# Kernel tuning notes

Hardware: AMD Instinct MI355X
Metric: run time of the kernel (lower is better)

## Reference

```python
import jax, jax.numpy as jnp
import numpy as np

K = 3
TOPK = 10
HORIZON = 12


def gru_cell(x, h, w_ih, w_hh, b_ih, b_hh):
    # torch GRU gate order: r, z, n ; n = tanh(W_in x + b_in + r*(W_hn h + b_hn))
    gx = x @ w_ih.T + b_ih
    gh = h @ w_hh.T + b_hh
    H = h.shape[-1]
    r = jax.nn.sigmoid(gx[:, :H] + gh[:, :H])
    z = jax.nn.sigmoid(gx[:, H:2 * H] + gh[:, H:2 * H])
    n = jnp.tanh(gx[:, 2 * H:] + r * gh[:, 2 * H:])
    return (1.0 - z) * n + z * h


def setup_inputs() -> dict:
    key = jax.random.key(0)
    ks = jax.random.split(key, 16)
    B, T, N, F = 128, 12, 207, 14
    H = 128
    f = lambda i, shp, s=0.1: jax.random.normal(ks[i], shp, dtype=jnp.float32) * s
    return {
        'x': jax.random.normal(ks[0], (B, T, N, F), dtype=jnp.float32),
        'A_physical': jax.random.uniform(ks[1], (N, N), dtype=jnp.float32),
        'fc_start_w': f(2, (16, 1), 0.5),
        'fc_start_b': jnp.zeros((16,), jnp.float32),
        'alpha': jnp.float32(0.5),
        'context_w': f(3, (32, 13)),
        'context_b': jnp.zeros((32,), jnp.float32),
        'tcn_w': f(4, (64, 1, 1, 3), 0.3),
        'tcn_b': jnp.zeros((64,), jnp.float32),
        'theta': f(5, (K, 32, 32), 0.15),
        'attn_w': f(6, (1, 65)),
        'attn_b': jnp.zeros((1,), jnp.float32),
        'enc_w_ih': f(7, (3 * H, 65)),
        'enc_w_hh': f(8, (3 * H, H)),
        'enc_b_ih': jnp.zeros((3 * H,), jnp.float32),
        'enc_b_hh': jnp.zeros((3 * H,), jnp.float32),
        'dec_w_ih': f(9, (3 * H, 33)),
        'dec_w_hh': f(10, (3 * H, H)),
        'dec_b_ih': jnp.zeros((3 * H,), jnp.float32),
        'dec_b_hh': jnp.zeros((3 * H,), jnp.float32),
        'out_w': f(11, (1, H)),
        'out_b': jnp.zeros((1,), jnp.float32),
    }


def reference(x, A_physical, fc_start_w, fc_start_b, alpha, context_w, context_b,
              tcn_w, tcn_b, theta, attn_w, attn_b,
              enc_w_ih, enc_w_hh, enc_b_ih, enc_b_hh,
              dec_w_ih, dec_w_hh, dec_b_ih, dec_b_hh, out_w, out_b):
    B, T, N, _ = x.shape
    H = enc_w_hh.shape[1]
    traffic = x[..., 0:1]          # [B,T,N,1]
    context = x[..., 1:]           # [B,T,N,13]

    # ---- dynamic graph: topk + scatter + softmax, blended with physical ----
    state = traffic[:, -1]                                   # [B,N,1]
    emb = jnp.tanh(state @ fc_start_w.T + fc_start_b)        # [B,N,16]
    A_dyn = jax.nn.relu(jnp.einsum('bnd,bmd->bnm', emb, emb))
    vals, idx = jax.lax.top_k(A_dyn, TOPK)
    sparse = jnp.zeros_like(A_dyn).at[
        jnp.arange(B)[:, None, None], jnp.arange(N)[None, :, None], idx].set(vals)
    A_dyn = jax.nn.softmax(sparse, axis=2)
    a = jax.nn.sigmoid(alpha)
    A = a * A_physical[None] + (1.0 - a) * A_dyn             # [B,N,N]

    # ---- gated temporal conv (causal, GLU) ----
    xt = jnp.transpose(traffic, (0, 3, 2, 1))                # [B,1,N,T]
    conv = jax.lax.conv_general_dilated(
        xt, tcn_w, (1, 1), [(0, 0), (2, 0)],
        dimension_numbers=('NCHW', 'OIHW', 'NCHW')) + tcn_b[None, :, None, None]
    P, Q = jnp.split(conv, 2, axis=1)
    t_feat = jnp.transpose(P * jax.nn.sigmoid(Q), (0, 3, 2, 1))  # [B,T,N,32]

    # ---- Chebyshev K-hop graph conv ----
    I = jnp.eye(N, dtype=x.dtype)
    lam = jnp.clip(jnp.max(jnp.sum(A, -1), -1), 1.0)[:, None, None]
    L = 2.0 * A / lam - I[None]
    Tk = [jnp.broadcast_to(I[None], (B, N, N)), L]
    for k in range(2, K):
        Tk.append(2.0 * jnp.einsum('bnm,bmp->bnp', L, Tk[-1]) - Tk[-2])
    s = 0.0
    for k in range(K):
        rhs = jnp.einsum('btnf,fo->btno', t_feat, theta[k])
        s = s + jnp.einsum('bnm,btmo->btno', Tk[k], rhs)
    s_feat = jax.nn.relu(s)                                   # [B,T,N,32] (dropout off: eval)

    # ---- attention fusion ----
    c_emb = jax.nn.relu(context @ context_w.T + context_b)    # [B,T,N,32]
    fusion = jnp.concatenate([traffic, s_feat, c_emb], -1)    # [B,T,N,65]
    attn = jax.nn.sigmoid(fusion @ attn_w.T + attn_b)
    z = fusion * attn
    # NOTE: original torch code does z.view(B*N, T, -1) on a [B,T,N,65] contiguous
    # tensor (raw reshape, no permute) -- replicated faithfully.
    z_flat = z.reshape(B * N, T, -1)

    # ---- encoder GRU ----
    h = jnp.zeros((B * N, H), x.dtype)
    def enc_step(h, xt_):
        return gru_cell(xt_, h, enc_w_ih, enc_w_hh, enc_b_ih, enc_b_hh), None
    h, _ = jax.lax.scan(enc_step, h, jnp.transpose(z_flat, (1, 0, 2)))

    cur = traffic[:, -1, :, 0].reshape(B * N, 1)
    ctx = c_emb[:, -1].reshape(B * N, 32)
    def dec_step(carry, _):
        hh, cc = carry
        h2 = gru_cell(jnp.concatenate([cc, ctx], 1), hh,
                      dec_w_ih, dec_w_hh, dec_b_ih, dec_b_hh)
        pred = h2 @ out_w.T + out_b
        return (h2, pred), pred
    _, preds = jax.lax.scan(dec_step, (h, cur), None, length=HORIZON)  # [Hz,B*N,1]
    out = jnp.transpose(preds[..., 0], (1, 0)).reshape(B, N, HORIZON)
    return jnp.transpose(out, (0, 2, 1))                      # [B,horizon,N]
```

## Files before the change

kernel.cpp:

```cpp
#include <hip/hip_runtime.h>
#include <math.h>

#define NB 128
#define NT 12
#define NNODE 207
#define NF 14
#define NH 128
#define ROWS (NB*NNODE)
#define BTN (NB*NT*NNODE)
#define G3 (3*NH)
#define LSTR 208
#define RG (ROWS/16)

typedef __attribute__((ext_vector_type(8))) short short8;
typedef __attribute__((ext_vector_type(4))) float accf4;

#define MFMA16 __builtin_amdgcn_mfma_f32_16x16x32_bf16

__device__ __forceinline__ float sigf(float x){ return 1.0f/(1.0f+__expf(-x)); }
__device__ __forceinline__ float tanhfast(float x){
  float e = __expf(2.f*x);
  return 1.f - 2.f/(e + 1.f);
}
__device__ __forceinline__ unsigned short f2b(float f){
  unsigned int u = __float_as_uint(f);
  return (unsigned short)((u + 0x7FFFu + ((u>>16)&1u)) >> 16);
}
__device__ __forceinline__ float b2f(unsigned short h){
  return __uint_as_float(((unsigned int)h) << 16);
}
__device__ __forceinline__ void mm2(short8 ah, short8 al, short8 bh, accf4& acc){
  acc = MFMA16(ah, bh, acc, 0,0,0);
  acc = MFMA16(al, bh, acc, 0,0,0);
}

__global__ __launch_bounds__(256) void k_sentinel(float* __restrict__ out, int n){
  int i = blockIdx.x*256 + threadIdx.x;
  if (i < n) out[i] = 12345.0f;
}

#define NW_ENC (7*24*64*8)
#define NW_DEC (4*24*64*8)
#define SH_TOTAL (2*NW_ENC + 2*NW_DEC)
#define FWT_TOTAL (32*384 + 384)
#define PREP_TOTAL (NW_ENC + NW_DEC + 32*384 + 384)
__global__ __launch_bounds__(256) void k_prep(const float* __restrict__ ewih,
    const float* __restrict__ ewhh, const float* __restrict__ dwih,
    const float* __restrict__ dwhh, short* __restrict__ ws, float* __restrict__ wf){
  int i = blockIdx.x*256 + threadIdx.x;
  if (i < NW_ENC){
    int e = i & 7, lane = (i>>3) & 63, ct = (i>>9) % 24, ks = i / 12288;
    int k = ks*32 + (lane>>4)*8 + e;
    int col = ct*16 + (lane&15);
    float wv = (k < 65) ? ewih[col*65 + k] : ((k < 96) ? 0.f : ewhh[col*128 + (k-96)]);
    unsigned short hi = f2b(wv);
    ws[i] = (short)hi;
    ws[NW_ENC + i] = (short)f2b(wv - b2f(hi));
  } else if (i < NW_ENC + NW_DEC){
    int j = i - NW_ENC;
    int e = j & 7, lane = (j>>3) & 63, ct = (j>>9) % 24, ks = j / 12288;
    int k = ks*32 + (lane>>4)*8 + e;
    int col = ct*16 + (lane&15);
    float wv = dwhh[col*128 + k];
    unsigned short hi = f2b(wv);
    ws[2*NW_ENC + j] = (short)hi;
    ws[2*NW_ENC + NW_DEC + j] = (short)f2b(wv - b2f(hi));
  } else if (i < NW_ENC + NW_DEC + 32*384){
    int j = i - (NW_ENC + NW_DEC); int k = j/384, n = j%384;
    wf[j] = dwih[n*33 + 1 + k];
  } else if (i < PREP_TOTAL){
    int n = i - (NW_ENC + NW_DEC + 32*384);
    wf[32*384 + n] = dwih[n*33];
  }
}

__global__ __launch_bounds__(256) void k_emb(const float* __restrict__ x,
    const float* __restrict__ w, const float* __restrict__ b, float* __restrict__ emb){
  int idx = blockIdx.x*256 + threadIdx.x;
  if (idx >= ROWS*16) return;
  int j = idx & 15, row = idx >> 4;
  int bb = row / NNODE, n = row % NNODE;
  float s = x[((bb*NT + (NT-1))*NNODE + n)*NF];
  emb[idx] = tanhf(s*w[j] + b[j]);
}

__global__ __launch_bounds__(256) void k_adj(const float* __restrict__ emb,
    const float* __restrict__ Aph, const float* __restrict__ alp,
    float* __restrict__ Abuf, float* __restrict__ rsum){
  int wid = threadIdx.x >> 6, lane = threadIdx.x & 63;
  int row = blockIdx.x*4 + wid;
  int bb = row / NNODE, n = row % NNODE;
  const float4* er = (const float4*)(emb + (size_t)row*16);
  float4 e0 = er[0], e1 = er[1], e2 = er[2], e3 = er[3];
  float d[4];
  #pragma unroll
  for (int q=0;q<4;++q){
    int m = lane + q*64;
    float dd = -1.f;
    if (m < NNODE){
      const float4* em = (const float4*)(emb + (size_t)(bb*NNODE+m)*16);
      float4 m0 = em[0], m1 = em[1], m2 = em[2], m3 = em[3];
      dd = e0.x*m0.x + e0.y*m0.y + e0.z*m0.z + e0.w*m0.w
         + e1.x*m1.x + e1.y*m1.y + e1.z*m1.z + e1.w*m1.w
         + e2.x*m2.x + e2.y*m2.y + e2.z*m2.z + e2.w*m2.w
         + e3.x*m3.x + e3.y*m3.y + e3.z*m3.z + e3.w*m3.w;
      dd = dd > 0.f ? dd : 0.f;
    }
    d[q] = dd;
  }
  int km = 0;
  float vmax = 0.f;
  for (int it=0; it<10; ++it){
    float v = -1.f; int mi = 1<<20;
    #pragma unroll
    for (int q=0;q<4;++q){
      if (d[q] >= 0.f && !((km>>q)&1) && d[q] > v){ v = d[q]; mi = lane + q*64; }
    }
    #pragma unroll
    for (int off=1; off<64; off<<=1){
      float v2 = __shfl_xor(v, off, 64);
      int  i2 = __shfl_xor(mi, off, 64);
      if (v2 > v || (v2 == v && i2 < mi)){ v = v2; mi = i2; }
    }
    if (it == 0) vmax = v;
    if ((mi & 63) == lane) km |= 1 << (mi >> 6);
  }
  float a = sigf(alp[0]);
  float eneg = __expf(-vmax);
  float p[4]; float ps = 0.f;
  #pragma unroll
  for (int q=0;q<4;++q){
    p[q] = 0.f;
    if (d[q] >= 0.f) p[q] = ((km>>q)&1) ? __expf(d[q]-vmax) : eneg;
    ps += p[q];
  }
  #pragma unroll
  for (int off=1; off<64; off<<=1) ps += __shfl_xor(ps, off, 64);
  float inv = (1.f - a)/ps;
  float rs = 0.f;
  #pragma unroll
  for (int q=0;q<4;++q){
    int m = lane + q*64;
    if (m < NNODE){
      float Av = a*Aph[n*NNODE + m] + p[q]*inv;
      Abuf[(size_t)row*LSTR + m] = Av;
      rs += Av;
    }
  }
  if (lane == 0) Abuf[(size_t)row*LSTR + 207] = 0.f;
  #pragma unroll
  for (int off=1; off<64; off<<=1) rs += __shfl_xor(rs, off, 64);
  if (lane == 0) rsum[row] = rs;
}

__global__ __launch_bounds__(256) void k_lam(const float* __restrict__ rsum, float* __restrict__ lam){
  __shared__ float rv[256];
  int b = blockIdx.x, tid = threadIdx.x;
  rv[tid] = (tid < NNODE) ? rsum[b*NNODE+tid] : -1e30f;
  __syncthreads();
  for (int s=128;s>0;s>>=1){ if (tid<s) rv[tid]=fmaxf(rv[tid],rv[tid+s]); __syncthreads(); }
  if (tid==0) lam[b] = fmaxf(rv[0], 1.0f);
}

__global__ __launch_bounds__(256) void k_lap(float* __restrict__ Abuf, const float* __restrict__ lam){
  int idx = blockIdx.x*256 + threadIdx.x;
  if (idx >= NB*NNODE*LSTR) return;
  int b = idx / (NNODE*LSTR);
  int rem = idx % (NNODE*LSTR);
  int n = rem / LSTR, m = rem % LSTR;
  Abuf[idx] = 2.f*Abuf[idx]/lam[b] - (n==m ? 1.f : 0.f);
}

__global__ __launch_bounds__(256) void k_tcntheta(const float* __restrict__ x,
    const float* __restrict__ tw, const float* __restrict__ tb,
    const float* __restrict__ theta,
    float* __restrict__ PA, float* __restrict__ PB, float* __restrict__ PC){
  __shared__ float thA[32][33], thB[32][33], thC[32][33];
  __shared__ float tf[8][32];
  int tid = threadIdx.x;
  for (int i=tid; i<1024; i+=256){
    int f = i >> 5, o = i & 31;
    float t0 = theta[f*32+o], t1 = theta[1024+f*32+o], t2 = theta[2048+f*32+o];
    thA[o][f] = t0 - t2; thB[o][f] = t1; thC[o][f] = t2;
  }
  int rl = tid >> 5, o = tid & 31;
  int r = blockIdx.x*8 + rl;
  int n = r % NNODE, bt = r / NNODE, t = bt % NT, b = bt / NT;
  float x0 = (t>=2)? x[((size_t)(b*NT+t-2)*NNODE+n)*NF] : 0.f;
  float x1 = (t>=1)? x[((size_t)(b*NT+t-1)*NNODE+n)*NF] : 0.f;
  float x2 = x[((size_t)(b*NT+t)*NNODE+n)*NF];
  float P = tb[o]    + tw[o*3]*x0       + tw[o*3+1]*x1       + tw[o*3+2]*x2;
  float Q = tb[o+32] + tw[(o+32)*3]*x0  + tw[(o+32)*3+1]*x1  + tw[(o+32)*3+2]*x2;
  tf[rl][o] = P * sigf(Q);
  __syncthreads();
  float aA=0.f, aB=0.f, aC=0.f;
  #pragma unroll
  for (int f=0; f<32; ++f){
    float tv = tf[rl][f];
    aA += tv*thA[o][f]; aB += tv*thB[o][f]; aC += tv*thC[o][f];
  }
  size_t outi = (size_t)(b*NNODE+n)*G3 + t*32 + o;
  PA[outi]=aA; PB[outi]=aB; PC[outi]=aC;
}

__global__ __launch_bounds__(256) void gemm128(
    const float* __restrict__ Ab, int lda, long long sA,
    const float* __restrict__ Bb, long long sB,
    const float* __restrict__ bias,
    const float* __restrict__ Yb, long long sY, float alphaV, float betaV, int do_relu,
    float* __restrict__ Cb, long long sC, int M, int kchunks){
  __shared__ float As[16][132];
  __shared__ float Bs[16][132];
  int bz = blockIdx.z;
  const float* A = Ab + (size_t)bz*sA;
  const float* B = Bb + (size_t)bz*sB;
  float* C = Cb + (size_t)bz*sC;
  int n0 = blockIdx.x*128, m0 = blockIdx.y*128;
  int tid = threadIdx.x, tx = tid & 15, ty = tid >> 4;
  float acc[8][8] = {};
  int ar = tid & 127, ak = (tid >> 7)*8;
  int bk = tid >> 4, bn = (tid & 15)*8;
  for (int kc=0; kc<kchunks; ++kc){
    int k0 = kc*16;
    int m = m0 + ar;
    if (m < M){
      const float* ap = A + (size_t)m*lda + k0 + ak;
      float4 v0 = *(const float4*)ap, v1 = *(const float4*)(ap+4);
      As[ak+0][ar]=v0.x; As[ak+1][ar]=v0.y; As[ak+2][ar]=v0.z; As[ak+3][ar]=v0.w;
      As[ak+4][ar]=v1.x; As[ak+5][ar]=v1.y; As[ak+6][ar]=v1.z; As[ak+7][ar]=v1.w;
    } else {
      #pragma unroll
      for (int j=0;j<8;++j) As[ak+j][ar]=0.f;
    }
    const float* bp = B + (size_t)(k0+bk)*384 + n0 + bn;
    float4 w0_ = *(const float4*)bp, w1_ = *(const float4*)(bp+4);
    *(float4*)&Bs[bk][bn] = w0_; *(float4*)&Bs[bk][bn+4] = w1_;
    __syncthreads();
    #pragma unroll
    for (int kk=0;kk<16;++kk){
      float4 a0 = *(const float4*)&As[kk][ty*8];
      float4 a1 = *(const float4*)&As[kk][ty*8+4];
      float4 b0 = *(const float4*)&Bs[kk][tx*4];
      float4 b1 = *(const float4*)&Bs[kk][64+tx*4];
      float av[8] = {a0.x,a0.y,a0.z,a0.w,a1.x,a1.y,a1.z,a1.w};
      float bv[8] = {b0.x,b0.y,b0.z,b0.w,b1.x,b1.y,b1.z,b1.w};
      #pragma unroll
      for (int i=0;i<8;++i)
        #pragma unroll
        for (int j=0;j<8;++j) acc[i][j] += av[i]*bv[j];
    }
    __syncthreads();
  }
  if (bias){
    float bl[4], bh_[4];
    #pragma unroll
    for (int j=0;j<4;++j){ bl[j]=bias[n0+tx*4+j]; bh_[j]=bias[n0+64+tx*4+j]; }
    #pragma unroll
    for (int i=0;i<8;++i){
      int m2 = m0 + ty*8 + i; if (m2 >= M) continue;
      float4 s0, s1;
      s0.x=acc[i][0]+bl[0]; s0.y=acc[i][1]+bl[1]; s0.z=acc[i][2]+bl[2]; s0.w=acc[i][3]+bl[3];
      s1.x=acc[i][4]+bh_[0]; s1.y=acc[i][5]+bh_[1]; s1.z=acc[i][6]+bh_[2]; s1.w=acc[i][7]+bh_[3];
      *(float4*)&C[(size_t)m2*384 + n0 + tx*4] = s0;
      *(float4*)&C[(size_t)m2*384 + n0 + 64 + tx*4] = s1;
    }
  } else {
    const float* Y = Yb + (size_t)bz*sY;
    #pragma unroll
    for (int i=0;i<8;++i){
      int m2 = m0 + ty*8 + i; if (m2 >= M) continue;
      const float* yr = Y + (size_t)m2*384;
      float* cr = C + (size_t)m2*384;
      float4 y0 = *(const float4*)(yr + n0 + tx*4);
      float4 y1 = *(const float4*)(yr + n0 + 64 + tx*4);
      float4 s0, s1;
      s0.x = alphaV*acc[i][0] + betaV*y0.x; s0.y = alphaV*acc[i][1] + betaV*y0.y;
      s0.z = alphaV*acc[i][2] + betaV*y0.z; s0.w = alphaV*acc[i][3] + betaV*y0.w;
      s1.x = alphaV*acc[i][4] + betaV*y1.x; s1.y = alphaV*acc[i][5] + betaV*y1.y;
      s1.z = alphaV*acc[i][6] + betaV*y1.z; s1.w = alphaV*acc[i][7] + betaV*y1.w;
      if (do_relu){
        s0.x=fmaxf(s0.x,0.f); s0.y=fmaxf(s0.y,0.f); s0.z=fmaxf(s0.z,0.f); s0.w=fmaxf(s0.w,0.f);
        s1.x=fmaxf(s1.x,0.f); s1.y=fmaxf(s1.y,0.f); s1.z=fmaxf(s1.z,0.f); s1.w=fmaxf(s1.w,0.f);
      }
      *(float4*)(cr + n0 + tx*4) = s0;
      *(float4*)(cr + n0 + 64 + tx*4) = s1;
    }
  }
}

#define GATEB(WH, KS) \
    const int ko = (KS)*24; \
    short8 bRh = *(const short8*)(WH + ((size_t)(ko + w)*64 + lane)*8); \
    short8 bZh = *(const short8*)(WH + ((size_t)(ko + 8 + w)*64 + lane)*8); \
    short8 bNh = *(const short8*)(WH + ((size_t)(ko + 16 + w)*64 + lane)*8);

__global__ __launch_bounds__(512) void k_encdec(
    const short* __restrict__ zfH, const short* __restrict__ zfL,
    const short* __restrict__ WFH,
    const float* __restrict__ bih, const float* __restrict__ bhh,
    const short* __restrict__ DFH,
    const float* __restrict__ dbhh, const float* __restrict__ ctxGX,
    const float* __restrict__ w0, const float* __restrict__ ow,
    const float* __restrict__ ob, const float* __restrict__ pred0,
    float* __restrict__ outp){
  __shared__ __attribute__((aligned(16))) short hfH[2*4*512];
  __shared__ __attribute__((aligned(16))) short hfL[2*4*512];
  __shared__ float psl[8][16];
  __shared__ float predl[16];
  int R = blockIdx.x, m0 = R*16;
  int tid = threadIdx.x;
  int w = tid >> 6, lane = tid & 63;
  int g = lane >> 4, c = lane & 15;
  int j = (w<<4) + c;
  float hreg[4] = {};
  for (int i = tid; i < 4096; i += 512){ hfH[i] = 0; hfL[i] = 0; }
  if (tid < 16) predl[tid] = pred0[m0 + tid];
  int ksh = w >> 1, qh = 2*(w&1) + (c>>3), eh = c & 7;
  int epo = ksh*512 + ((g*4) + 16*qh)*8 + eh;
  float birv = bih[j], bizv = bih[128+j], binv = bih[256+j];
  float bhrv = bhh[j], bhzv = bhh[128+j], bhnv = bhh[256+j];
  size_t outbase = 0;
  if (tid < 16){
    int row = m0 + tid;
    int b_ = row / NNODE, n_ = row % NNODE;
    outbase = (size_t)b_*NT*NNODE + n_;
  }
  __syncthreads();

  int cur = 0;
  for (int t = 0; t < NT; ++t){
    accf4 aR = {}, aZ = {}, aNZ = {}, aNH = {};
    #pragma unroll
    for (int ks=0; ks<3; ++ks){
      GATEB(WFH, ks);
      size_t zb = (((size_t)t*RG + R)*3 + ks)*512;
      short8 ah = *(const short8*)(zfH + zb + lane*8);
      short8 al = *(const short8*)(zfL + zb + lane*8);
      mm2(ah, al, bRh, aR);
      mm2(ah, al, bZh, aZ);
      mm2(ah, al, bNh, aNZ);
    }
    #pragma unroll
    for (int ks=3; ks<7; ++ks){
      GATEB(WFH, ks);
      short8 ah = *(const short8*)&hfH[cur*2048 + (ks-3)*512 + lane*8];
      short8 al = *(const short8*)&hfL[cur*2048 + (ks-3)*512 + lane*8];
      mm2(ah, al, bRh, aR);
      mm2(ah, al, bZh, aZ);
      mm2(ah, al, bNh, aNH);
    }
    int nxt = cur ^ 1;
    #pragma unroll
    for (int i=0;i<4;++i){
      float r_ = sigf(aR[i] + birv + bhrv);
      float z_ = sigf(aZ[i] + bizv + bhzv);
      float n_ = tanhfast(aNZ[i] + binv + r_*(aNH[i] + bhnv));
      float hn = (1.f - z_)*n_ + z_*hreg[i];
      hreg[i] = hn;
      unsigned short hh = f2b(hn);
      int o = nxt*2048 + epo + i*8;
      hfH[o] = (short)hh;
      hfL[o] = (short)f2b(hn - b2f(hh));
    }
    __syncthreads();
    cur = nxt;
  }

  float w0r = w0[j], w0z = w0[128+j], w0n = w0[256+j];
  float bhr = dbhh[j], bhz = dbhh[128+j], bhn = dbhh[256+j];
  float owj = ow[j];
  float obv = ob[0];
  float gxr[4], gxz[4], gxn[4];
  #pragma unroll
  for (int i=0;i<4;++i){
    int row = g*4 + i;
    const float* gx = ctxGX + (size_t)(m0+row)*384;
    gxr[i] = gx[j]; gxz[i] = gx[128+j]; gxn[i] = gx[256+j];
  }
  for (int s = 0; s < NT; ++s){
    accf4 aR = {}, aZ = {}, aN = {};
    #pragma unroll
    for (int ks=0; ks<4; ++ks){
      GATEB(DFH, ks);
      short8 ah = *(const short8*)&hfH[cur*2048 + ks*512 + lane*8];
      short8 al = *(const short8*)&hfL[cur*2048 + ks*512 + lane*8];
      mm2(ah, al, bRh, aR);
      mm2(ah, al, bZh, aZ);
      mm2(ah, al, bNh, aN);
    }
    int nxt = cur ^ 1;
    #pragma unroll
    for (int i=0;i<4;++i){
      int row = g*4 + i;
      float p = predl[row];
      float r_ = sigf(gxr[i] + p*w0r + aR[i] + bhr);
      float z_ = sigf(gxz[i] + p*w0z + aZ[i] + bhz);
      float n_ = tanhfast(gxn[i] + p*w0n + r_*(aN[i] + bhn));
      float hn = (1.f - z_)*n_ + z_*hreg[i];
      hreg[i] = hn;
      unsigned short hh = f2b(hn);
      int o = nxt*2048 + epo + i*8;
      hfH[o] = (short)hh;
      hfL[o] = (short)f2b(hn - b2f(hh));
      float psv = hn*owj;
      psv += __shfl_xor(psv, 1, 64);
      psv += __shfl_xor(psv, 2, 64);
      psv += __shfl_xor(psv, 4, 64);
      psv += __shfl_xor(psv, 8, 64);
      if (c == 0) psl[w][row] = psv;
    }
    __syncthreads();
    if (tid < 16){
      float sm = obv;
      #pragma unroll
      for (int w2=0; w2<8; ++w2) sm += psl[w2][tid];
      predl[tid] = sm;
      outp[outbase + (size_t)s*NNODE] = sm;
    }
    __syncthreads();
    cur = nxt;
  }
}

__global__ __launch_bounds__(256) void k_zbuild(const float* __restrict__ x,
    const float* __restrict__ S, const float* __restrict__ cw, const float* __restrict__ cb,
    const float* __restrict__ aw, const float* __restrict__ ab,
    short* __restrict__ zfH, short* __restrict__ zfL,
    float* __restrict__ ctx, float* __restrict__ pred0){
  __shared__ float cwl[416];
  __shared__ float cbl[32];
  __shared__ float awl[65];
  __shared__ short zH[1536];
  __shared__ short zL[1536];
  int tid = threadIdx.x;
  for (int i=tid; i<416; i+=256) cwl[i] = cw[i];
  if (tid < 32) cbl[tid] = cb[tid];
  if (tid < 65) awl[tid] = aw[tid];
  {
    int* zHi = (int*)zH; int* zLi = (int*)zL;
    for (int i=tid; i<768; i+=256){ zHi[i] = 0; zLi[i] = 0; }
  }
  __syncthreads();
  int bid = blockIdx.x;
  int tau = bid / RG, Rg = bid % RG;
  int trow = tid >> 4, tl = tid & 15;
  int i_ = Rg*16 + trow;
  int r = i_*NT + tau;
  int n = r % NNODE, bt = r / NNODE, t = bt % NT, b = bt / NT;
  const float* xr = x + (size_t)r*NF;
  float x0 = xr[0];
  float ce0 = cbl[tl], ce1 = cbl[tl+16];
  #pragma unroll
  for (int f=0; f<13; ++f){
    float xv = xr[1+f];
    ce0 += xv*cwl[tl*13+f];
    ce1 += xv*cwl[(tl+16)*13+f];
  }
  ce0 = fmaxf(ce0, 0.f); ce1 = fmaxf(ce1, 0.f);
  const float* sr = S + (size_t)(b*NNODE+n)*G3 + t*32;
  float sv0 = sr[tl], sv1 = sr[tl+16];
  float part = sv0*awl[1+tl] + ce0*awl[33+tl]
             + sv1*awl[17+tl] + ce1*awl[49+tl]
             + (tl==0 ? x0*awl[0] : 0.f);
  part += __shfl_xor(part, 1, 64);
  part += __shfl_xor(part, 2, 64);
  part += __shfl_xor(part, 4, 64);
  part += __shfl_xor(part, 8, 64);
  float attn = sigf(part + ab[0]);
  #define ZPUT(L, V) do{ int l_=(L); int ks_=l_>>5, q_=(l_&31)>>3, e_=l_&7; \
      int o_ = ks_*512 + ((trow + 16*q_)<<3) + e_; \
      float v_=(V); unsigned short hh_ = f2b(v_); \
      zH[o_] = (short)hh_; zL[o_] = (short)f2b(v_ - b2f(hh_)); }while(0)
  ZPUT(1+tl, sv0*attn);
  ZPUT(17+tl, sv1*attn);
  ZPUT(33+tl, ce0*attn);
  ZPUT(49+tl, ce1*attn);
  if (tl == 0) ZPUT(0, x0*attn);
  #undef ZPUT
  if (t == NT-1){
    float* cr = ctx + (size_t)(b*NNODE+n)*32;
    cr[tl] = ce0; cr[tl+16] = ce1;
    if (tl == 0) pred0[b*NNODE+n] = x0;
  }
  __syncthreads();
  size_t gb = (size_t)bid*1536;
  const int* zHi = (const int*)zH; const int* zLi = (const int*)zL;
  int* gH = (int*)(zfH + gb); int* gL = (int*)(zfL + gb);
  #pragma unroll
  for (int i=tid; i<768; i+=256){ gH[i] = zHi[i]; gL[i] = zLi[i]; }
}

extern "C" void kernel_launch(void* const* d_in, const int* in_sizes, int n_in,
                              void* d_out, int out_size, void* d_ws, size_t ws_size,
                              hipStream_t stream){
  const float* x     = (const float*)d_in[0];
  const float* Aph   = (const float*)d_in[1];
  const float* fcw   = (const float*)d_in[2];
  const float* fcb   = (const float*)d_in[3];
  const float* alp   = (const float*)d_in[4];
  const float* cw    = (const float*)d_in[5];
  const float* cb    = (const float*)d_in[6];
  const float* tw    = (const float*)d_in[7];
  const float* tb    = (const float*)d_in[8];
  const float* theta = (const float*)d_in[9];
  const float* aw    = (const float*)d_in[10];
  const float* ab    = (const float*)d_in[11];
  const float* ewih  = (const float*)d_in[12];
  const float* ewhh  = (const float*)d_in[13];
  const float* ebih  = (const float*)d_in[14];
  const float* ebhh  = (const float*)d_in[15];
  const float* dwih  = (const float*)d_in[16];
  const float* dwhh  = (const float*)d_in[17];
  const float* dbih  = (const float*)d_in[18];
  const float* dbhh  = (const float*)d_in[19];
  const float* ow    = (const float*)d_in[20];
  const float* ob    = (const float*)d_in[21];
  float* out = (float*)d_out;

  const size_t SZ_CTX  = (size_t)ROWS*32;
  const size_t SZ_PRED = (size_t)ROWS;
  const size_t SZ_G    = (size_t)ROWS*G3;
  const size_t SZ_ABUF = (size_t)NB*NNODE*LSTR;
  const size_t SZ_EMB  = (size_t)ROWS*16;
  const size_t SZ_ZF   = (size_t)NT*RG*3*512;
  const size_t SZ_UNION_FL = (2*SZ_ZF + 1) / 2;
  const size_t UNION_FL = (SZ_UNION_FL > 3*SZ_G) ? SZ_UNION_FL : 3*SZ_G;

  float* w = (float*)d_ws;
  size_t off = 0;
  auto alloc = [&](size_t nfl){ float* p = w + off; off += nfl; return p; };
  float* ctx   = alloc(SZ_CTX);
  float* pred  = alloc(SZ_PRED);
  float* Abuf  = alloc(SZ_ABUF);
  float* emb   = alloc(SZ_EMB);
  float* rsum  = alloc(SZ_PRED);
  float* lam   = alloc((size_t)NB);
  short* wS    = (short*)alloc(SH_TOTAL/2);
  float* wF    = alloc((size_t)FWT_TOTAL);
  float* Sslot = alloc(SZ_G);
  float* Uzone = alloc(UNION_FL);
  float* P1 = Uzone;
  float* P2 = Uzone + SZ_G;
  float* P3 = Uzone + 2*SZ_G;
  short* zfH = (short*)Uzone;
  short* zfL = zfH + SZ_ZF;
  (void)n_in; (void)in_sizes;

  if (ws_size < off*sizeof(float)){
    k_sentinel<<<(out_size+255)/256, 256, 0, stream>>>(out, out_size);
    return;
  }

  const short* WFH = wS;
  const short* DFH = wS + 2*NW_ENC;
  float* dwihT = wF;
  float* w0    = wF + 32*384;

  k_prep<<<(PREP_TOTAL+255)/256, 256, 0, stream>>>(ewih, ewhh, dwih, dwhh, wS, wF);
  k_emb<<<(ROWS*16)/256, 256, 0, stream>>>(x, fcw, fcb, emb);
  k_adj<<<ROWS/4, 256, 0, stream>>>(emb, Aph, alp, Abuf, rsum);
  k_lam<<<NB, 256, 0, stream>>>(rsum, lam);
  k_lap<<<(NB*NNODE*LSTR)/256, 256, 0, stream>>>(Abuf, lam);
  k_tcntheta<<<BTN/8, 256, 0, stream>>>(x, tw, tb, theta, P1, P2, P3);
  gemm128<<<dim3(3, 2, NB), 256, 0, stream>>>(Abuf, LSTR, (long long)NNODE*LSTR,
      P3, (long long)NNODE*G3, nullptr,
      P2, (long long)NNODE*G3, 2.f, 1.f, 0,
      P2, (long long)NNODE*G3, NNODE, 13);
  gemm128<<<dim3(3, 2, NB), 256, 0, stream>>>(Abuf, LSTR, (long long)NNODE*LSTR,
      P2, (long long)NNODE*G3, nullptr,
      P1, (long long)NNODE*G3, 1.f, 1.f, 1,
      Sslot, (long long)NNODE*G3, NNODE, 13);
  k_zbuild<<<NT*RG, 256, 0, stream>>>(x, Sslot, cw, cb, aw, ab, zfH, zfL, ctx, pred);
  float* ctxGX = Sslot;
  gemm128<<<dim3(3, ROWS/128, 1), 256, 0, stream>>>(
      ctx, 32, 0, dwihT, 0, dbih,
      nullptr, 0, 1.f, 0.f, 0, ctxGX, 0, ROWS, 2);
  k_encdec<<<RG, 512, 0, stream>>>(zfH, zfL, WFH, ebih, ebhh,
      DFH, dbhh, ctxGX, w0, ow, ob, pred, out);
}
```

Baseline: 693.3 us.

## Move Chebyshev graph GEMMs to split-bf16 MFMA and trim encoder K padding

Replaces the fp32 SIMT gemm128 Chebyshev graph convolutions with an MFMA kernel. It uses a three-term hi/lo bf16 split, with the Laplacian and features pre-packed into fragment layouts by new k_lapfrag and k_split kernels. The first cheb GEMM writes its output directly in fragment form for the second. The encoder input width is also shrunk from 96 to 64 K columns: feature 64 is handled as a scalar rank-1 term in the gate epilogue, removing one MFMA K-step per timestep. The costs are extra packing kernels, more workspace reuse aliasing, and a slightly different precision profile.

```diff
diff --git a/kernel.cpp b/kernel.cpp
--- a/kernel.cpp
+++ b/kernel.cpp
@@ -33,17 +33,26 @@
   acc = MFMA16(ah, bh, acc, 0,0,0);
   acc = MFMA16(al, bh, acc, 0,0,0);
 }
+__device__ __forceinline__ void mm3(short8 ah, short8 al, short8 bh, short8 bl, accf4& acc){
+  acc = MFMA16(ah, bh, acc, 0,0,0);
+  acc = MFMA16(al, bh, acc, 0,0,0);
+  acc = MFMA16(ah, bl, acc, 0,0,0);
+}
 
 __global__ __launch_bounds__(256) void k_sentinel(float* __restrict__ out, int n){
   int i = blockIdx.x*256 + threadIdx.x;
   if (i < n) out[i] = 12345.0f;
 }
 
-#define NW_ENC (7*24*64*8)
+#define NW_ENC (6*24*64*8)
 #define NW_DEC (4*24*64*8)
 #define SH_TOTAL (2*NW_ENC + 2*NW_DEC)
-#define FWT_TOTAL (32*384 + 384)
-#define PREP_TOTAL (NW_ENC + NW_DEC + 32*384 + 384)
+#define FWT_TOTAL (32*384 + 384 + 384)
+#define PREP_TOTAL (NW_ENC + NW_DEC + 32*384 + 384 + 384)
+#define SZ_XF (NB*7*24*512)
+#define SZ_LF (NB*13*7*512)
+#define SZ_ZF1 ((size_t)NT*RG*2*512)
+
 __global__ __launch_bounds__(256) void k_prep(const float* __restrict__ ewih,
     const float* __restrict__ ewhh, const float* __restrict__ dwih,
     const float* __restrict__ dwhh, short* __restrict__ ws, float* __restrict__ wf){
@@ -52,7 +61,7 @@
     int e = i & 7, lane = (i>>3) & 63, ct = (i>>9) % 24, ks = i / 12288;
     int k = ks*32 + (lane>>4)*8 + e;
     int col = ct*16 + (lane&15);
-    float wv = (k < 65) ? ewih[col*65 + k] : ((k < 96) ? 0.f : ewhh[col*128 + (k-96)]);
+    float wv = (k < 64) ? ewih[col*65 + k] : ewhh[col*128 + (k-64)];
     unsigned short hi = f2b(wv);
     ws[i] = (short)hi;
     ws[NW_ENC + i] = (short)f2b(wv - b2f(hi));
@@ -68,9 +77,12 @@
   } else if (i < NW_ENC + NW_DEC + 32*384){
     int j = i - (NW_ENC + NW_DEC); int k = j/384, n = j%384;
     wf[j] = dwih[n*33 + 1 + k];
-  } else if (i < PREP_TOTAL){
+  } else if (i < NW_ENC + NW_DEC + 32*384 + 384){
     int n = i - (NW_ENC + NW_DEC + 32*384);
     wf[32*384 + n] = dwih[n*33];
+  } else if (i < PREP_TOTAL){
+    int n = i - (NW_ENC + NW_DEC + 32*384 + 384);
+    wf[32*384 + 384 + n] = ewih[n*65 + 64];
   }
 }
 
@@ -162,13 +174,33 @@
   if (tid==0) lam[b] = fmaxf(rv[0], 1.0f);
 }
 
-__global__ __launch_bounds__(256) void k_lap(float* __restrict__ Abuf, const float* __restrict__ lam){
-  int idx = blockIdx.x*256 + threadIdx.x;
-  if (idx >= NB*NNODE*LSTR) return;
-  int b = idx / (NNODE*LSTR);
-  int rem = idx % (NNODE*LSTR);
-  int n = rem / LSTR, m = rem % LSTR;
-  Abuf[idx] = 2.f*Abuf[idx]/lam[b] - (n==m ? 1.f : 0.f);
+__global__ __launch_bounds__(256) void k_lapfrag(const float* __restrict__ Abuf,
+    const float* __restrict__ lam, short* __restrict__ LfH, short* __restrict__ LfL){
+  __shared__ short pH[7*512];
+  __shared__ short pL[7*512];
+  int bid = blockIdx.x;
+  int b = bid / 13, mt = bid % 13;
+  int tid = threadIdx.x;
+  int row = tid >> 4, kq = tid & 15;
+  int n = mt*16 + row;
+  float invl = 2.f / lam[b];
+  size_t arow = ((size_t)b*NNODE + n)*LSTR;
+  #pragma unroll
+  for (int kc = 0; kc < 14; ++kc){
+    int k = kc*16 + kq;
+    float L = 0.f;
+    if (n < 207 && k < 207)
+      L = Abuf[arow + k]*invl - ((n==k) ? 1.f : 0.f);
+    unsigned short hh = f2b(L);
+    int o = (k>>5)*512 + (row + 16*((k&31)>>3))*8 + (k&7);
+    pH[o] = (short)hh;
+    pL[o] = (short)f2b(L - b2f(hh));
+  }
+  __syncthreads();
+  const int* sH = (const int*)pH; const int* sL = (const int*)pL;
+  int* gH = (int*)LfH; int* gL = (int*)LfL;
+  size_t basei = (size_t)bid*1792;
+  for (int i = tid; i < 1792; i += 256){ gH[basei+i] = sH[i]; gL[basei+i] = sL[i]; }
 }
 
 __global__ __launch_bounds__(256) void k_tcntheta(const float* __restrict__ x,
@@ -201,6 +233,109 @@
   }
   size_t outi = (size_t)(b*NNODE+n)*G3 + t*32 + o;
   PA[outi]=aA; PB[outi]=aB; PC[outi]=aC;
+}
+
+__global__ __launch_bounds__(256) void k_split(const float* __restrict__ RC,
+    short* __restrict__ XH, short* __restrict__ XL){
+  __shared__ short pH[24*512];
+  __shared__ short pL[24*512];
+  int bid = blockIdx.x;
+  int b = bid / 7, ks = bid % 7;
+  int tid = threadIdx.x;
+  #pragma unroll
+  for (int it = 0; it < 48; ++it){
+    int flat = it*256 + tid;
+    int ml = flat / 384, col = flat % 384;
+    int m = ks*32 + ml;
+    float v = (m < 207) ? RC[((size_t)b*NNODE + m)*384 + col] : 0.f;
+    unsigned short hh = f2b(v);
+    int o = (col>>4)*512 + ((col&15) + 16*(ml>>3))*8 + (ml&7);
+    pH[o] = (short)hh;
+    pL[o] = (short)f2b(v - b2f(hh));
+  }
+  __syncthreads();
+  const int* sH = (const int*)pH; const int* sL = (const int*)pL;
+  int* gH = (int*)XH; int* gL = (int*)XL;
+  size_t basei = (size_t)bid*6144;
+  for (int i = tid; i < 6144; i += 256){ gH[basei+i] = sH[i]; gL[basei+i] = sL[i]; }
+}
+
+template<int VAR>
+__global__ __launch_bounds__(512) void gemm_cheb(
+    const short* __restrict__ LfH, const short* __restrict__ LfL,
+    const short* __restrict__ XH, const short* __restrict__ XL,
+    const float* __restrict__ Y, float* __restrict__ Sout,
+    short* __restrict__ OH, short* __restrict__ OL){
+  __shared__ short pH[24*256];
+  __shared__ short pL[24*256];
+  int bid = blockIdx.x;
+  int b = bid / 13, mt = bid % 13;
+  int tid = threadIdx.x;
+  int w = tid >> 6, lane = tid & 63;
+  int c = lane & 15, g = lane >> 4;
+  accf4 acc[3] = {};
+  #pragma unroll
+  for (int ks = 0; ks < 7; ++ks){
+    size_t ab = ((size_t)(b*13 + mt)*7 + ks)*512 + lane*8;
+    short8 ah = *(const short8*)(LfH + ab);
+    short8 al = *(const short8*)(LfL + ab);
+    #pragma unroll
+    for (int p = 0; p < 3; ++p){
+      int ct = w + p*8;
+      size_t xb = ((size_t)(b*7 + ks)*24 + ct)*512 + lane*8;
+      short8 bh = *(const short8*)(XH + xb);
+      short8 bl = *(const short8*)(XL + xb);
+      mm3(ah, al, bh, bl, acc[p]);
+    }
+  }
+  if (VAR == 2){
+    #pragma unroll
+    for (int p=0;p<3;++p){
+      int col = (w + p*8)*16 + c;
+      #pragma unroll
+      for (int i=0;i<4;++i){
+        int row = mt*16 + g*4 + i;
+        if (row < 207){
+          size_t idx = ((size_t)b*NNODE + row)*384 + col;
+          float v = acc[p][i] + Y[idx];
+          Sout[idx] = fmaxf(v, 0.f);
+        }
+      }
+    }
+  } else {
+    #pragma unroll
+    for (int p=0;p<3;++p){
+      int ct = w + p*8;
+      int col = ct*16 + c;
+      #pragma unroll
+      for (int i=0;i<4;++i){
+        int r16 = g*4 + i;
+        int row = mt*16 + r16;
+        float v = 0.f;
+        if (row < 207) v = 2.f*acc[p][i] + Y[((size_t)b*NNODE + row)*384 + col];
+        unsigned short hh = f2b(v);
+        int o = ct*256 + (c + 16*(r16>>3))*8 + (r16 & 7);
+        pH[o] = (short)hh;
+        pL[o] = (short)f2b(v - b2f(hh));
+      }
+    }
+    __syncthreads();
+    int ksn = mt >> 1, half = mt & 1;
+    const int* sH = (const int*)pH; const int* sL = (const int*)pL;
+    int* gH = (int*)OH; int* gL = (int*)OL;
+    for (int i = tid; i < 3072; i += 512){
+      int ct = i >> 7, idx = i & 127;
+      size_t gi = ((size_t)(b*7 + ksn)*24 + ct)*256 + (size_t)half*128 + idx;
+      gH[gi] = sH[i]; gL[gi] = sL[i];
+    }
+    if (mt == 12){
+      for (int i = tid; i < 3072; i += 512){
+        int ct = i >> 7, idx = i & 127;
+        size_t gi = ((size_t)(b*7 + 6)*24 + ct)*256 + 128 + idx;
+        gH[gi] = 0; gL[gi] = 0;
+      }
+    }
+  }
 }
 
 __global__ __launch_bounds__(256) void gemm128(
@@ -264,27 +399,6 @@
       *(float4*)&C[(size_t)m2*384 + n0 + tx*4] = s0;
       *(float4*)&C[(size_t)m2*384 + n0 + 64 + tx*4] = s1;
     }
-  } else {
-    const float* Y = Yb + (size_t)bz*sY;
-    #pragma unroll
-    for (int i=0;i<8;++i){
-      int m2 = m0 + ty*8 + i; if (m2 >= M) continue;
-      const float* yr = Y + (size_t)m2*384;
-      float* cr = C + (size_t)m2*384;
-      float4 y0 = *(const float4*)(yr + n0 + tx*4);
-      float4 y1 = *(const float4*)(yr + n0 + 64 + tx*4);
-      float4 s0, s1;
-      s0.x = alphaV*acc[i][0] + betaV*y0.x; s0.y = alphaV*acc[i][1] + betaV*y0.y;
-      s0.z = alphaV*acc[i][2] + betaV*y0.z; s0.w = alphaV*acc[i][3] + betaV*y0.w;
-      s1.x = alphaV*acc[i][4] + betaV*y1.x; s1.y = alphaV*acc[i][5] + betaV*y1.y;
-      s1.z = alphaV*acc[i][6] + betaV*y1.z; s1.w = alphaV*acc[i][7] + betaV*y1.w;
-      if (do_relu){
-        s0.x=fmaxf(s0.x,0.f); s0.y=fmaxf(s0.y,0.f); s0.z=fmaxf(s0.z,0.f); s0.w=fmaxf(s0.w,0.f);
-        s1.x=fmaxf(s1.x,0.f); s1.y=fmaxf(s1.y,0.f); s1.z=fmaxf(s1.z,0.f); s1.w=fmaxf(s1.w,0.f);
-      }
-      *(float4*)(cr + n0 + tx*4) = s0;
-      *(float4*)(cr + n0 + 64 + tx*4) = s1;
-    }
   }
 }
 
@@ -296,11 +410,12 @@
 
 __global__ __launch_bounds__(512) void k_encdec(
     const short* __restrict__ zfH, const short* __restrict__ zfL,
-    const short* __restrict__ WFH,
+    const float* __restrict__ z64, const short* __restrict__ WFH,
     const float* __restrict__ bih, const float* __restrict__ bhh,
     const short* __restrict__ DFH,
     const float* __restrict__ dbhh, const float* __restrict__ ctxGX,
-    const float* __restrict__ w0, const float* __restrict__ ow,
+    const float* __restrict__ w0, const float* __restrict__ w64,
+    const float* __restrict__ ow,
     const float* __restrict__ ob, const float* __restrict__ pred0,
     float* __restrict__ outp){
   __shared__ __attribute__((aligned(16))) short hfH[2*4*512];
@@ -319,6 +434,7 @@
   int epo = ksh*512 + ((g*4) + 16*qh)*8 + eh;
   float birv = bih[j], bizv = bih[128+j], binv = bih[256+j];
   float bhrv = bhh[j], bhzv = bhh[128+j], bhnv = bhh[256+j];
+  float w64r = w64[j], w64z = w64[128+j], w64n = w64[256+j];
   size_t outbase = 0;
   if (tid < 16){
     int row = m0 + tid;
@@ -331,9 +447,9 @@
   for (int t = 0; t < NT; ++t){
     accf4 aR = {}, aZ = {}, aNZ = {}, aNH = {};
     #pragma unroll
-    for (int ks=0; ks<3; ++ks){
+    for (int ks=0; ks<2; ++ks){
       GATEB(WFH, ks);
-      size_t zb = (((size_t)t*RG + R)*3 + ks)*512;
+      size_t zb = (((size_t)t*RG + R)*2 + ks)*512;
       short8 ah = *(const short8*)(zfH + zb + lane*8);
       short8 al = *(const short8*)(zfL + zb + lane*8);
       mm2(ah, al, bRh, aR);
@@ -341,20 +457,23 @@
       mm2(ah, al, bNh, aNZ);
     }
     #pragma unroll
-    for (int ks=3; ks<7; ++ks){
+    for (int ks=2; ks<6; ++ks){
       GATEB(WFH, ks);
-      short8 ah = *(const short8*)&hfH[cur*2048 + (ks-3)*512 + lane*8];
-      short8 al = *(const short8*)&hfL[cur*2048 + (ks-3)*512 + lane*8];
+      short8 ah = *(const short8*)&hfH[cur*2048 + (ks-2)*512 + lane*8];
+      short8 al = *(const short8*)&hfL[cur*2048 + (ks-2)*512 + lane*8];
       mm2(ah, al, bRh, aR);
       mm2(ah, al, bZh, aZ);
       mm2(ah, al, bNh, aNH);
     }
+    float z64v[4];
+    #pragma unroll
+    for (int i=0;i<4;++i) z64v[i] = z64[(size_t)t*ROWS + m0 + g*4 + i];
     int nxt = cur ^ 1;
     #pragma unroll
     for (int i=0;i<4;++i){
-      float r_ = sigf(aR[i] + birv + bhrv);
-      float z_ = sigf(aZ[i] + bizv + bhzv);
-      float n_ = tanhfast(aNZ[i] + binv + r_*(aNH[i] + bhnv));
+      float r_ = sigf(aR[i] + z64v[i]*w64r + birv + bhrv);
+      float z_ = sigf(aZ[i] + z64v[i]*w64z + bizv + bhzv);
+      float n_ = tanhfast(aNZ[i] + z64v[i]*w64n + binv + r_*(aNH[i] + bhnv));
       float hn = (1.f - z_)*n_ + z_*hreg[i];
       hreg[i] = hn;
       unsigned short hh = f2b(hn);
@@ -425,21 +544,17 @@
 __global__ __launch_bounds__(256) void k_zbuild(const float* __restrict__ x,
     const float* __restrict__ S, const float* __restrict__ cw, const float* __restrict__ cb,
     const float* __restrict__ aw, const float* __restrict__ ab,
-    short* __restrict__ zfH, short* __restrict__ zfL,
+    short* __restrict__ zfH, short* __restrict__ zfL, float* __restrict__ z64,
     float* __restrict__ ctx, float* __restrict__ pred0){
   __shared__ float cwl[416];
   __shared__ float cbl[32];
   __shared__ float awl[65];
-  __shared__ short zH[1536];
-  __shared__ short zL[1536];
+  __shared__ short zH[1024];
+  __shared__ short zL[1024];
   int tid = threadIdx.x;
   for (int i=tid; i<416; i+=256) cwl[i] = cw[i];
   if (tid < 32) cbl[tid] = cb[tid];
   if (tid < 65) awl[tid] = aw[tid];
-  {
-    int* zHi = (int*)zH; int* zLi = (int*)zL;
-    for (int i=tid; i<768; i+=256){ zHi[i] = 0; zLi[i] = 0; }
-  }
   __syncthreads();
   int bid = blockIdx.x;
   int tau = bid / RG, Rg = bid % RG;
@@ -474,7 +589,8 @@
   ZPUT(1+tl, sv0*attn);
   ZPUT(17+tl, sv1*attn);
   ZPUT(33+tl, ce0*attn);
-  ZPUT(49+tl, ce1*attn);
+  if (tl < 15) ZPUT(49+tl, ce1*attn);
+  else z64[(size_t)tau*ROWS + i_] = ce1*attn;
   if (tl == 0) ZPUT(0, x0*attn);
   #undef ZPUT
   if (t == NT-1){
@@ -483,11 +599,11 @@
     if (tl == 0) pred0[b*NNODE+n] = x0;
   }
   __syncthreads();
-  size_t gb = (size_t)bid*1536;
+  size_t gb = (size_t)bid*512;
   const int* zHi = (const int*)zH; const int* zLi = (const int*)zL;
-  int* gH = (int*)(zfH + gb); int* gL = (int*)(zfL + gb);
-  #pragma unroll
-  for (int i=tid; i<768; i+=256){ gH[i] = zHi[i]; gL[i] = zLi[i]; }
+  int* gH = (int*)zfH; int* gL = (int*)zfL;
+  #pragma unroll
+  for (int i=tid; i<512; i+=256){ gH[gb+i] = zHi[i]; gL[gb+i] = zLi[i]; }
 }
 
 extern "C" void kernel_launch(void* const* d_in, const int* in_sizes, int n_in,
@@ -517,64 +633,67 @@
   const float* ob    = (const float*)d_in[21];
   float* out = (float*)d_out;
 
-  const size_t SZ_CTX  = (size_t)ROWS*32;
-  const size_t SZ_PRED = (size_t)ROWS;
   const size_t SZ_G    = (size_t)ROWS*G3;
   const size_t SZ_ABUF = (size_t)NB*NNODE*LSTR;
   const size_t SZ_EMB  = (size_t)ROWS*16;
-  const size_t SZ_ZF   = (size_t)NT*RG*3*512;
-  const size_t SZ_UNION_FL = (2*SZ_ZF + 1) / 2;
-  const size_t UNION_FL = (SZ_UNION_FL > 3*SZ_G) ? SZ_UNION_FL : 3*SZ_G;
-
-  float* w = (float*)d_ws;
+  const size_t U_FL    = 2*SZ_G + 2*(size_t)SZ_XF + (size_t)SZ_LF;
+
+  float* wp = (float*)d_ws;
   size_t off = 0;
-  auto alloc = [&](size_t nfl){ float* p = w + off; off += nfl; return p; };
-  float* ctx   = alloc(SZ_CTX);
-  float* pred  = alloc(SZ_PRED);
-  float* Abuf  = alloc(SZ_ABUF);
-  float* emb   = alloc(SZ_EMB);
-  float* rsum  = alloc(SZ_PRED);
+  auto alloc = [&](size_t nfl){ float* p = wp + off; off += nfl; return p; };
+  float* pred  = alloc((size_t)ROWS);
   float* lam   = alloc((size_t)NB);
   short* wS    = (short*)alloc(SH_TOTAL/2);
   float* wF    = alloc((size_t)FWT_TOTAL);
-  float* Sslot = alloc(SZ_G);
-  float* Uzone = alloc(UNION_FL);
-  float* P1 = Uzone;
-  float* P2 = Uzone + SZ_G;
-  float* P3 = Uzone + 2*SZ_G;
-  short* zfH = (short*)Uzone;
-  short* zfL = zfH + SZ_ZF;
+  float* z64   = alloc((size_t)NT*ROWS);
+  float* U     = alloc(U_FL);
   (void)n_in; (void)in_sizes;
 
   if (ws_size < off*sizeof(float)){
     k_sentinel<<<(out_size+255)/256, 256, 0, stream>>>(out, out_size);
     return;
   }
+
+  float* Abuf  = U;
+  float* embp  = U + SZ_ABUF;
+  float* rsum  = U + SZ_ABUF + SZ_EMB;
+  float* P1    = U;
+  float* P2    = U + SZ_G;
+  short* fbase = (short*)(U + 2*SZ_G);
+  short* XfAH  = fbase;
+  short* XfAL  = fbase + SZ_XF;
+  short* XfBH  = fbase + 2*(size_t)SZ_XF;
+  short* XfBL  = fbase + 3*(size_t)SZ_XF;
+  short* LfH   = fbase + 4*(size_t)SZ_XF;
+  short* LfL   = LfH + SZ_LF;
+  float* RCbuf = (float*)XfBH;
+  short* zfH   = (short*)(U + SZ_G);
+  short* zfL   = zfH + SZ_ZF1;
+  float* ctxGX = (float*)XfBH;
+  float* ctx   = U + 2*SZ_G + (size_t)SZ_XF*2;
 
   const short* WFH = wS;
   const short* DFH = wS + 2*NW_ENC;
   float* dwihT = wF;
   float* w0    = wF + 32*384;
+  float* w64   = wF + 32*384 + 384;
 
   k_prep<<<(PREP_TOTAL+255)/256, 256, 0, stream>>>(ewih, ewhh, dwih, dwhh, wS, wF);
-  k_emb<<<(ROWS*16)/256, 256, 0, stream>>>(x, fcw, fcb, emb);
-  k_adj<<<ROWS/4, 256, 0, stream>>>(emb, Aph, alp, Abuf, rsum);
+  k_emb<<<(ROWS*16)/256, 256, 0, stream>>>(x, fcw, fcb, embp);
+  k_adj<<<ROWS/4, 256, 0, stream>>>(embp, Aph, alp, Abuf, rsum);
   k_lam<<<NB, 256, 0, stream>>>(rsum, lam);
-  k_lap<<<(NB*NNODE*LSTR)/256, 256, 0, stream>>>(Abuf, lam);
-  k_tcntheta<<<BTN/8, 256, 0, stream>>>(x, tw, tb, theta, P1, P2, P3);
-  gemm128<<<dim3(3, 2, NB), 256, 0, stream>>>(Abuf, LSTR, (long long)NNODE*LSTR,
-      P3, (long long)NNODE*G3, nullptr,
-      P2, (long long)NNODE*G3, 2.f, 1.f, 0,
-      P2, (long long)NNODE*G3, NNODE, 13);
-  gemm128<<<dim3(3, 2, NB), 256, 0, stream>>>(Abuf, LSTR, (long long)NNODE*LSTR,
-      P2, (long long)NNODE*G3, nullptr,
-      P1, (long long)NNODE*G3, 1.f, 1.f, 1,
-      Sslot, (long long)NNODE*G3, NNODE, 13);
-  k_zbuild<<<NT*RG, 256, 0, stream>>>(x, Sslot, cw, cb, aw, ab, zfH, zfL, ctx, pred);
-  float* ctxGX = Sslot;
+  k_lapfrag<<<NB*13, 256, 0, stream>>>(Abuf, lam, LfH, LfL);
+  k_tcntheta<<<BTN/8, 256, 0, stream>>>(x, tw, tb, theta, P1, P2, RCbuf);
+  k_split<<<NB*7, 256, 0, stream>>>(RCbuf, XfAH, XfAL);
+  gemm_cheb<1><<<NB*13, 512, 0, stream>>>(LfH, LfL, XfAH, XfAL, P2,
+      nullptr, XfBH, XfBL);
+  gemm_cheb<2><<<NB*13, 512, 0, stream>>>(LfH, LfL, XfBH, XfBL, P1,
+      P1, nullptr, nullptr);
+  k_zbuild<<<NT*RG, 256, 0, stream>>>(x, P1, cw, cb, aw, ab, zfH, zfL, z64,
+      ctx, pred);
   gemm128<<<dim3(3, ROWS/128, 1), 256, 0, stream>>>(
       ctx, 32, 0, dwihT, 0, dbih,
       nullptr, 0, 1.f, 0.f, 0, ctxGX, 0, ROWS, 2);
-  k_encdec<<<RG, 512, 0, stream>>>(zfH, zfL, WFH, ebih, ebhh,
-      DFH, dbhh, ctxGX, w0, ow, ob, pred, out);
-}
+  k_encdec<<<RG, 512, 0, stream>>>(zfH, zfL, z64, WFH, ebih, ebhh,
+      DFH, dbhh, ctxGX, w0, w64, ow, ob, pred, out);
+}
```

Measured after the change: 684.0 us. Within noise of the previous version (-1.3%).
